# Optimization experiments

Measured on AMD Instinct MI355X. Metric: run time of the kernel, lower is better.

Reference implementation:

```python
import jax, jax.numpy as jnp
import numpy as np

B, N, C_IN, C_OUT, BASIS = 8, 128, 64, 64, 15
AVG_NOBJ = 49.0
NEG_SLOPE = 0.01  # torch LeakyReLU default


def eops_2_to_2_sum(x, average_nobj=AVG_NOBJ):
    """x: [B, C, N, N] -> [B, C, 15, N, N].
    5 order-zero ops + 10 sum-aggregation ops (sums normalized by average_nobj,
    double sums by average_nobj**2, as in PELICAN's 'sum' aggregation)."""
    n = x.shape[-1]
    eye = jnp.eye(n, dtype=x.dtype)                       # [N, N]
    d = jnp.diagonal(x, axis1=-2, axis2=-1)               # [B, C, N]
    rowsum = x.sum(-1) / average_nobj                      # [B, C, N]
    colsum = x.sum(-2) / average_nobj                      # [B, C, N]
    trace = d.sum(-1) / average_nobj                       # [B, C]
    allsum = x.sum((-2, -1)) / (average_nobj ** 2)         # [B, C]
    bc = lambda v: jnp.broadcast_to(v, x.shape)
    ops = [
        # --- order zero (no aggregation) ---
        d[..., :, None] * eye,                 # diag(A) embedded on diagonal
        bc(d[..., :, None]),                   # A_ii broadcast along j
        bc(d[..., None, :]),                   # A_jj broadcast along i
        x,                                     # identity
        jnp.swapaxes(x, -1, -2),               # transpose
        # --- aggregation ops ---
        rowsum[..., :, None] * eye,            # row sums on diagonal
        colsum[..., :, None] * eye,            # col sums on diagonal
        trace[..., None, None] * eye,          # trace on diagonal
        allsum[..., None, None] * eye,         # total sum on diagonal
        bc(rowsum[..., :, None]),              # rowsum_i broadcast along j
        bc(rowsum[..., None, :]),              # rowsum_j broadcast along i
        bc(colsum[..., :, None]),              # colsum_i broadcast along j
        bc(colsum[..., None, :]),              # colsum_j broadcast along i
        bc(trace[..., None, None]),            # trace broadcast everywhere
        bc(allsum[..., None, None]),           # total sum broadcast everywhere
    ]
    return jnp.stack(ops, axis=2)              # [B, C, 15, N, N]


def setup_inputs() -> dict:
    key = jax.random.key(0)
    ks = jax.random.split(key, 5)
    inputs = jax.random.normal(ks[0], (B, N, N, C_IN), jnp.float32)
    mask = jnp.ones((B, N, N, 1), jnp.float32)
    nobj = jnp.full((B,), float(N), jnp.float32)
    s_b = float(np.sqrt(1.0 / BASIS))
    s_d = float(np.sqrt(1.0 / C_IN))
    coefs00 = jax.random.normal(ks[1], (C_IN, BASIS), jnp.float32) * s_b
    coefs01 = jax.random.normal(ks[2], (C_OUT, BASIS), jnp.float32) * s_b
    coefs10 = jax.random.normal(ks[3], (C_IN, C_OUT), jnp.float32) * s_d
    coefs11 = jax.random.normal(ks[4], (C_IN, C_OUT), jnp.float32) * s_d
    bias = jnp.zeros((C_OUT,), jnp.float32)
    diag_bias = jnp.zeros((C_OUT,), jnp.float32)
    return {"inputs": inputs, "mask": mask, "nobj": nobj,
            "coefs00": coefs00, "coefs01": coefs01,
            "coefs10": coefs10, "coefs11": coefs11,
            "bias": bias, "diag_bias": diag_bias}


def reference(inputs, mask, nobj, coefs00, coefs01, coefs10, coefs11, bias, diag_bias):
    # inputs: [B, N, N, C_in] -> channels-first for basis construction
    x = jnp.transpose(inputs, (0, 3, 1, 2))                     # [B, C, N, N]
    ops = eops_2_to_2_sum(x)                                    # [B, C, 15, N, N]
    # low-rank reconstructed coefficient tensor [C_in, C_out, 15]
    coefs = (coefs00[:, None, :] * coefs10[:, :, None]
             + coefs01[None, :, :] * coefs11[:, :, None])
    out = jnp.einsum('dsb,ndbij->nijs', coefs, ops)             # [B, N, N, C_out]
    eye = jnp.eye(inputs.shape[1], dtype=out.dtype)[None, :, :, None]
    out = out + bias[None, None, None, :] + eye * diag_bias[None, None, None, :]
    out = jax.nn.leaky_relu(out, NEG_SLOPE)
    return out * mask
```

## Files before the change

### kernel.cpp

```cpp
#include <hip/hip_runtime.h>

#define BB 8
#define NN 128
#define CC 64
static constexpr float INV_A = 1.0f / 49.0f;

#define OFF_C    0
#define OFF_CB   61440
#define OFF_RS   65536
#define OFF_CS   131072
#define OFF_DV   196608
#define OFF_U1   263168
#define OFF_U2   328704
#define OFF_DG   394240
#define OFF_XT   459776

typedef __attribute__((ext_vector_type(8))) short v8s;
typedef __attribute__((ext_vector_type(4))) float v4f;

static __device__ inline unsigned pack2bf(float a, float b) {
    union { float f; unsigned u; } ua, ub; ua.f = a; ub.f = b;
    return ((ua.u + 0x8000u) >> 16) | ((ub.u + 0x8000u) & 0xffff0000u);
}
static __device__ inline unsigned short f2bf(float a) {
    union { float f; unsigned u; } ua; ua.f = a;
    return (unsigned short)((ua.u + 0x8000u) >> 16);
}

__global__ void k_pre(const float* __restrict__ in,
                      const float* __restrict__ c00, const float* __restrict__ c01,
                      const float* __restrict__ c10, const float* __restrict__ c11,
                      float* __restrict__ ws) {
    if (blockIdx.x >= 512) {
        int idx = (blockIdx.x - 512) * 256 + threadIdx.x;
        if (idx < 15 * 4096) {
            int b = idx >> 12; int r = idx & 4095; int d = r >> 6; int s = r & 63;
            ws[OFF_C + idx] = c00[d * 15 + b] * c10[d * 64 + s] + c01[s * 15 + b] * c11[d * 64 + s];
        } else if (idx < 15 * 4096 + 8192) {
            int k = idx - 15 * 4096;
            int which = k >> 12;
            int r = k & 4095; int s = r >> 6; int d = r & 63;
            int b = 3 + which;
            float v = c00[d * 15 + b] * c10[d * 64 + s] + c01[s * 15 + b] * c11[d * 64 + s];
            unsigned short* cb = (unsigned short*)(ws + OFF_CB);
            cb[s * 128 + which * 64 + d] = f2bf(v);
        }
        return;
    }
    __shared__ float4 part[4][4][16];
    int mode = blockIdx.x >> 8;
    int bb = blockIdx.x & 255;
    int n = bb >> 5; int g0 = (bb & 31) * 4;
    int t = threadIdx.x;
    int q = t >> 6; int ii = (t >> 4) & 3; int d4 = t & 15;
    float4 acc = make_float4(0.f, 0.f, 0.f, 0.f);
    if (mode == 0) {
        int i = g0 + ii;
        float4 dvv = acc; bool hd = false;
        const float* base = in + ((size_t)(n * NN + i)) * NN * CC + d4 * 4;
        for (int j = q * 32; j < q * 32 + 32; ++j) {
            float4 v = *(const float4*)(base + (size_t)j * CC);
            acc.x += v.x; acc.y += v.y; acc.z += v.z; acc.w += v.w;
            if (j == i) { dvv = v; hd = true; }
        }
        if (hd) *(float4*)(ws + OFF_DV + ((size_t)(n * NN + i)) * CC + d4 * 4) = dvv;
    } else {
        int j = g0 + ii;
        unsigned short* xT = (unsigned short*)(ws + OFF_XT);
        for (int i = q * 32; i < q * 32 + 32; ++i) {
            float4 v = *(const float4*)(in + (((size_t)(n * NN + i)) * NN + j) * CC + d4 * 4);
            acc.x += v.x; acc.y += v.y; acc.z += v.z; acc.w += v.w;
            uint2 pk; pk.x = pack2bf(v.x, v.y); pk.y = pack2bf(v.z, v.w);
            *(uint2*)(xT + (((size_t)(n * NN + j)) * NN + i) * CC + d4 * 4) = pk;
        }
    }
    part[q][ii][d4] = acc;
    __syncthreads();
    if (t < 64) {
        int i2 = t >> 4; int dd = t & 15;
        float4 a = part[0][i2][dd], b = part[1][i2][dd], c = part[2][i2][dd], d = part[3][i2][dd];
        float4 s;
        s.x = (a.x + b.x + c.x + d.x) * INV_A;
        s.y = (a.y + b.y + c.y + d.y) * INV_A;
        s.z = (a.z + b.z + c.z + d.z) * INV_A;
        s.w = (a.w + b.w + c.w + d.w) * INV_A;
        *(float4*)(ws + (mode ? OFF_CS : OFF_RS) + ((size_t)(n * NN + g0 + i2)) * CC + dd * 4) = s;
    }
}

__global__ __launch_bounds__(256, 4) void k_uv(const float* __restrict__ bias,
                                               const float* __restrict__ dbias,
                                               float* __restrict__ ws) {
    __shared__ float trL[64], asL[64];
    __shared__ float pU1[4][4][64], pU2[4][4][64], pDG[4][4][64];
    __shared__ float pS[4][64], pDGc[4][64];
    int n = blockIdx.x >> 5; int i0 = (blockIdx.x & 31) * 4;
    int t = threadIdx.x;
    int s = t & 63; int q = t >> 6;

    {
        float tr = 0.f, as = 0.f;
        #pragma unroll 4
        for (int e = 0; e < 32; ++e) {
            int i = q * 32 + e;
            tr += ws[OFF_DV + ((size_t)(n * NN + i)) * CC + s];
            as += ws[OFF_RS + ((size_t)(n * NN + i)) * CC + s];
        }
        pS[q][s] = tr; pDGc[q][s] = as;
        __syncthreads();
        if (t < 64) {
            trL[t] = (pS[0][t] + pS[1][t] + pS[2][t] + pS[3][t]) * INV_A;
            asL[t] = (pDGc[0][t] + pDGc[1][t] + pDGc[2][t] + pDGc[3][t]) * INV_A;
        }
        __syncthreads();
    }

    const float* C = ws + OFF_C;
    float aU1[4] = {0, 0, 0, 0}, aU2[4] = {0, 0, 0, 0}, aDG[4] = {0, 0, 0, 0};
    float aS = 0.f, aDGc = 0.f;
    #pragma unroll
    for (int c4 = 0; c4 < 4; ++c4) {
        int dc = q * 4 + c4;
        float tr4[4], as4[4], dv4[4][4], rs4[4][4], cs4[4][4];
        #pragma unroll
        for (int k = 0; k < 4; ++k) { tr4[k] = trL[dc * 4 + k]; as4[k] = asL[dc * 4 + k]; }
        #pragma unroll
        for (int ii = 0; ii < 4; ++ii) {
            size_t ro = ((size_t)(n * NN + i0 + ii)) * CC + dc * 4;
            float4 v = *(const float4*)(ws + OFF_DV + ro);
            dv4[ii][0] = v.x; dv4[ii][1] = v.y; dv4[ii][2] = v.z; dv4[ii][3] = v.w;
            float4 r = *(const float4*)(ws + OFF_RS + ro);
            rs4[ii][0] = r.x; rs4[ii][1] = r.y; rs4[ii][2] = r.z; rs4[ii][3] = r.w;
            float4 c = *(const float4*)(ws + OFF_CS + ro);
            cs4[ii][0] = c.x; cs4[ii][1] = c.y; cs4[ii][2] = c.z; cs4[ii][3] = c.w;
        }
        #pragma unroll
        for (int k = 0; k < 4; ++k) {
            int d = dc * 4 + k;
            const float* Cd = C + d * 64 + s;
            float c0 = Cd[0 * 4096], c1 = Cd[1 * 4096], c2 = Cd[2 * 4096];
            float c5 = Cd[5 * 4096], c6 = Cd[6 * 4096], c7 = Cd[7 * 4096];
            float c8 = Cd[8 * 4096], c9 = Cd[9 * 4096], c10v = Cd[10 * 4096];
            float c11v = Cd[11 * 4096], c12v = Cd[12 * 4096];
            float c13 = Cd[13 * 4096], c14 = Cd[14 * 4096];
            aS += c13 * tr4[k] + c14 * as4[k];
            aDGc += c7 * tr4[k] + c8 * as4[k];
            #pragma unroll
            for (int ii = 0; ii < 4; ++ii) {
                aU1[ii] += c1 * dv4[ii][k] + c9 * rs4[ii][k] + c11v * cs4[ii][k];
                aU2[ii] += c2 * dv4[ii][k] + c10v * rs4[ii][k] + c12v * cs4[ii][k];
                aDG[ii] += c0 * dv4[ii][k] + c5 * rs4[ii][k] + c6 * cs4[ii][k];
            }
        }
    }
    #pragma unroll
    for (int ii = 0; ii < 4; ++ii) {
        pU1[q][ii][s] = aU1[ii]; pU2[q][ii][s] = aU2[ii]; pDG[q][ii][s] = aDG[ii];
    }
    pS[q][s] = aS; pDGc[q][s] = aDGc;
    __syncthreads();

    int fi = q;
    float u1 = pU1[0][fi][s] + pU1[1][fi][s] + pU1[2][fi][s] + pU1[3][fi][s];
    float u2 = pU2[0][fi][s] + pU2[1][fi][s] + pU2[2][fi][s] + pU2[3][fi][s];
    float dg = pDG[0][fi][s] + pDG[1][fi][s] + pDG[2][fi][s] + pDG[3][fi][s];
    float aSt = pS[0][s] + pS[1][s] + pS[2][s] + pS[3][s];
    float aDGct = pDGc[0][s] + pDGc[1][s] + pDGc[2][s] + pDGc[3][s];
    size_t row = ((size_t)(n * NN + i0 + fi)) * CC + s;
    ws[OFF_U1 + row] = u1 + aSt + bias[s];
    ws[OFF_U2 + row] = u2;
    ws[OFF_DG + row] = dg + aDGct + dbias[s];
}

__global__ __launch_bounds__(256, 4) void k_main(
        const float* __restrict__ in, const float* __restrict__ mask,
        const float* __restrict__ ws, float* __restrict__ out) {
    __shared__ __align__(16) unsigned char smem[34816];
    unsigned short* Ab = (unsigned short*)smem;
    unsigned short* Bb = (unsigned short*)(smem + 17408);
    float* Obuf = (float*)smem;

    int blk = blockIdx.x;
    int n = blk >> 8; int rem = blk & 255; int i = rem >> 1; int j0 = (rem & 1) * 64;
    int t = threadIdx.x;
    int tp = t >> 4; int c = t & 15;

    const unsigned short* cb = (const unsigned short*)(ws + OFF_CB);
    #pragma unroll
    for (int e = 0; e < 4; ++e) {
        int s = e * 16 + tp;
        float4 v = *(const float4*)(cb + s * 128 + c * 8);
        *(float4*)((unsigned char*)(Bb + s * 136 + c * 8)) = v;
    }
    {
        const float* src = in + (((size_t)(n * NN + i)) * NN + j0) * CC;
        #pragma unroll
        for (int e = 0; e < 4; ++e) {
            int p = e * 16 + tp;
            float4 v = *(const float4*)(src + (size_t)p * CC + c * 4);
            uint2 pk; pk.x = pack2bf(v.x, v.y); pk.y = pack2bf(v.z, v.w);
            *(uint2*)(Ab + p * 136 + c * 4) = pk;
        }
    }
    {
        const unsigned short* xT = (const unsigned short*)(ws + OFF_XT)
                                 + (((size_t)(n * NN + i)) * NN + j0) * CC;
        #pragma unroll
        for (int r = 0; r < 2; ++r) {
            int idx = t + r * 256;
            int p = idx >> 3; int ch = idx & 7;
            float4 v = *(const float4*)(xT + (size_t)p * CC + ch * 8);
            *(float4*)((unsigned char*)(Ab + p * 136 + 64 + ch * 8)) = v;
        }
    }
    __syncthreads();

    int w = t >> 6; int l = t & 63;
    int r16 = l & 15; int quad = l >> 4;
    v4f acc[4];
    #pragma unroll
    for (int st = 0; st < 4; ++st) acc[st] = 0.f;
    int arow = w * 16 + r16;
    #pragma unroll
    for (int kk = 0; kk < 4; ++kk) {
        v8s af = *(const v8s*)(Ab + arow * 136 + kk * 32 + quad * 8);
        #pragma unroll
        for (int st = 0; st < 4; ++st) {
            v8s bfr = *(const v8s*)(Bb + (st * 16 + r16) * 136 + kk * 32 + quad * 8);
            acc[st] = __builtin_amdgcn_mfma_f32_16x16x32_bf16(af, bfr, acc[st], 0, 0, 0);
        }
    }
    #pragma unroll
    for (int st = 0; st < 4; ++st)
        #pragma unroll
        for (int reg = 0; reg < 4; ++reg)
            Obuf[(w * 16 + quad * 4 + reg) * 68 + st * 16 + r16] = acc[st][reg];
    __syncthreads();

    int srow = (n * NN + i) * CC;
    float4 u1 = *(const float4*)(ws + OFF_U1 + srow + c * 4);
    float4 dg = *(const float4*)(ws + OFF_DG + srow + c * 4);
    #pragma unroll
    for (int e = 0; e < 4; ++e) {
        int p = e * 16 + tp;
        int j = j0 + p;
        float4 v = *(const float4*)(Obuf + p * 68 + c * 4);
        float4 u2 = *(const float4*)(ws + OFF_U2 + (n * NN + j) * CC + c * 4);
        v.x += u1.x + u2.x; v.y += u1.y + u2.y; v.z += u1.z + u2.z; v.w += u1.w + u2.w;
        if (j == i) { v.x += dg.x; v.y += dg.y; v.z += dg.z; v.w += dg.w; }
        v.x = v.x > 0.f ? v.x : 0.01f * v.x;
        v.y = v.y > 0.f ? v.y : 0.01f * v.y;
        v.z = v.z > 0.f ? v.z : 0.01f * v.z;
        v.w = v.w > 0.f ? v.w : 0.01f * v.w;
        float m = mask[((size_t)(n * NN + i)) * NN + j];
        v.x *= m; v.y *= m; v.z *= m; v.w *= m;
        *(float4*)(out + (((size_t)(n * NN + i)) * NN + j) * CC + c * 4) = v;
    }
}

extern "C" void kernel_launch(void* const* d_in, const int* in_sizes, int n_in,
                              void* d_out, int out_size, void* d_ws, size_t ws_size,
                              hipStream_t stream) {
    const float* inputs = (const float*)d_in[0];
    const float* mask   = (const float*)d_in[1];
    const float* c00 = (const float*)d_in[3];
    const float* c01 = (const float*)d_in[4];
    const float* c10 = (const float*)d_in[5];
    const float* c11 = (const float*)d_in[6];
    const float* bias  = (const float*)d_in[7];
    const float* dbias = (const float*)d_in[8];
    float* out = (float*)d_out;
    float* ws = (float*)d_ws;

    k_pre <<<784, 256, 0, stream>>>(inputs, c00, c01, c10, c11, ws);
    k_uv  <<<256, 256, 0, stream>>>(bias, dbias, ws);
    k_main<<<2048, 256, 0, stream>>>(inputs, mask, ws, out);
}
```

Before: 135.5 us.

## Fuse row and column sum passes into single input read with atomic row sums

The pre-pass used to read the input twice, once for row sums and diagonal and once for column sums and the bf16 transpose. It now reads it once per column block, computing column sums in shared memory and row sums through wavefront shuffles plus float atomics into a zeroed buffer. This halves global input traffic in the pre-pass but adds an extra zeroing kernel launch and many atomic adds, which also make the row-sum order nondeterministic.

```diff
diff --git a/kernel.cpp b/kernel.cpp
--- a/kernel.cpp
+++ b/kernel.cpp
@@ -27,12 +27,19 @@
     return (unsigned short)((ua.u + 0x8000u) >> 16);
 }
 
+__global__ void k_zero(float* __restrict__ ws) {
+    int idx = blockIdx.x * 256 + threadIdx.x;
+    float4 z = make_float4(0.f, 0.f, 0.f, 0.f);
+    *(float4*)(ws + OFF_RS + (size_t)idx * 4) = z;
+}
+
 __global__ void k_pre(const float* __restrict__ in,
                       const float* __restrict__ c00, const float* __restrict__ c01,
                       const float* __restrict__ c10, const float* __restrict__ c11,
                       float* __restrict__ ws) {
-    if (blockIdx.x >= 512) {
-        int idx = (blockIdx.x - 512) * 256 + threadIdx.x;
+    int t = threadIdx.x;
+    if (blockIdx.x >= 256) {
+        int idx = (blockIdx.x - 256) * 512 + t;
         if (idx < 15 * 4096) {
             int b = idx >> 12; int r = idx & 4095; int d = r >> 6; int s = r & 63;
             ws[OFF_C + idx] = c00[d * 15 + b] * c10[d * 64 + s] + c01[s * 15 + b] * c11[d * 64 + s];
@@ -47,44 +54,52 @@
         }
         return;
     }
-    __shared__ float4 part[4][4][16];
-    int mode = blockIdx.x >> 8;
-    int bb = blockIdx.x & 255;
-    int n = bb >> 5; int g0 = (bb & 31) * 4;
-    int t = threadIdx.x;
-    int q = t >> 6; int ii = (t >> 4) & 3; int d4 = t & 15;
+    __shared__ float4 part[8][4][16];
+    int n = blockIdx.x >> 5; int g0 = (blockIdx.x & 31) * 4;
+    int q  = t >> 6;
+    int ii = (t >> 4) & 3;
+    int d4 = t & 15;
+    int j = g0 + ii;
+
+    const float* src0 = in + ((size_t)(n * NN) * NN + j) * CC + d4 * 4;
+    unsigned short* xT = (unsigned short*)(ws + OFF_XT)
+                       + ((size_t)(n * NN + j)) * NN * CC + d4 * 4;
+    float* rsbase = ws + OFF_RS + (size_t)(n * NN) * CC + d4 * 4;
+
     float4 acc = make_float4(0.f, 0.f, 0.f, 0.f);
-    if (mode == 0) {
-        int i = g0 + ii;
-        float4 dvv = acc; bool hd = false;
-        const float* base = in + ((size_t)(n * NN + i)) * NN * CC + d4 * 4;
-        for (int j = q * 32; j < q * 32 + 32; ++j) {
-            float4 v = *(const float4*)(base + (size_t)j * CC);
-            acc.x += v.x; acc.y += v.y; acc.z += v.z; acc.w += v.w;
-            if (j == i) { dvv = v; hd = true; }
-        }
-        if (hd) *(float4*)(ws + OFF_DV + ((size_t)(n * NN + i)) * CC + d4 * 4) = dvv;
-    } else {
-        int j = g0 + ii;
-        unsigned short* xT = (unsigned short*)(ws + OFF_XT);
-        for (int i = q * 32; i < q * 32 + 32; ++i) {
-            float4 v = *(const float4*)(in + (((size_t)(n * NN + i)) * NN + j) * CC + d4 * 4);
-            acc.x += v.x; acc.y += v.y; acc.z += v.z; acc.w += v.w;
-            uint2 pk; pk.x = pack2bf(v.x, v.y); pk.y = pack2bf(v.z, v.w);
-            *(uint2*)(xT + (((size_t)(n * NN + j)) * NN + i) * CC + d4 * 4) = pk;
+    #pragma unroll 4
+    for (int e = 0; e < 16; ++e) {
+        int i = q * 16 + e;
+        float4 v = *(const float4*)(src0 + (size_t)i * NN * CC);
+        acc.x += v.x; acc.y += v.y; acc.z += v.z; acc.w += v.w;
+        uint2 pk; pk.x = pack2bf(v.x, v.y); pk.y = pack2bf(v.z, v.w);
+        *(uint2*)(xT + (size_t)i * CC) = pk;
+        if (i == j) *(float4*)(ws + OFF_DV + ((size_t)(n * NN + i)) * CC + d4 * 4) = v;
+        float sx = v.x, sy = v.y, sz = v.z, sw = v.w;
+        sx += __shfl_xor(sx, 16); sy += __shfl_xor(sy, 16);
+        sz += __shfl_xor(sz, 16); sw += __shfl_xor(sw, 16);
+        sx += __shfl_xor(sx, 32); sy += __shfl_xor(sy, 32);
+        sz += __shfl_xor(sz, 32); sw += __shfl_xor(sw, 32);
+        if (ii == 0) {
+            float* p = rsbase + (size_t)i * CC;
+            atomicAdd(p + 0, sx * INV_A);
+            atomicAdd(p + 1, sy * INV_A);
+            atomicAdd(p + 2, sz * INV_A);
+            atomicAdd(p + 3, sw * INV_A);
         }
     }
     part[q][ii][d4] = acc;
     __syncthreads();
     if (t < 64) {
-        int i2 = t >> 4; int dd = t & 15;
-        float4 a = part[0][i2][dd], b = part[1][i2][dd], c = part[2][i2][dd], d = part[3][i2][dd];
-        float4 s;
-        s.x = (a.x + b.x + c.x + d.x) * INV_A;
-        s.y = (a.y + b.y + c.y + d.y) * INV_A;
-        s.z = (a.z + b.z + c.z + d.z) * INV_A;
-        s.w = (a.w + b.w + c.w + d.w) * INV_A;
-        *(float4*)(ws + (mode ? OFF_CS : OFF_RS) + ((size_t)(n * NN + g0 + i2)) * CC + dd * 4) = s;
+        int jj = t >> 4; int dd = t & 15;
+        float4 s = make_float4(0.f, 0.f, 0.f, 0.f);
+        #pragma unroll
+        for (int qq = 0; qq < 8; ++qq) {
+            float4 a = part[qq][jj][dd];
+            s.x += a.x; s.y += a.y; s.z += a.z; s.w += a.w;
+        }
+        s.x *= INV_A; s.y *= INV_A; s.z *= INV_A; s.w *= INV_A;
+        *(float4*)(ws + OFF_CS + ((size_t)(n * NN + g0 + jj)) * CC + dd * 4) = s;
     }
 }
 
@@ -272,7 +287,8 @@
     float* out = (float*)d_out;
     float* ws = (float*)d_ws;
 
-    k_pre <<<784, 256, 0, stream>>>(inputs, c00, c01, c10, c11, ws);
+    k_zero<<<64, 256, 0, stream>>>(ws);
+    k_pre <<<392, 512, 0, stream>>>(inputs, c00, c01, c10, c11, ws);
     k_uv  <<<256, 256, 0, stream>>>(bias, dbias, ws);
     k_main<<<2048, 256, 0, stream>>>(inputs, mask, ws, out);
 }
```

New measurement: 173.0 us. 1.28x slower.
